# Kernel tuning notes

Hardware: AMD Instinct MI355X
Metric: run time of the kernel (lower is better)

The kernel has to match this reference:

```python
import jax, jax.numpy as jnp
import numpy as np

D_MODEL = 1024
N_HEADS = 16
HEAD_DIM = D_MODEL // N_HEADS
B, L = 2, 2048


def setup_inputs() -> dict:
    key = jax.random.key(0)
    ks = jax.random.split(key, 9)
    s = 1.0 / np.sqrt(D_MODEL)
    return {
        "hidden_states": jax.random.normal(ks[0], (B, L, D_MODEL), dtype=jnp.float32),
        "Wq": jax.random.uniform(ks[1], (D_MODEL, D_MODEL), jnp.float32, -s, s),
        "bq": jax.random.uniform(ks[2], (D_MODEL,), jnp.float32, -s, s),
        "Wk": jax.random.uniform(ks[3], (D_MODEL, D_MODEL), jnp.float32, -s, s),
        "bk": jax.random.uniform(ks[4], (D_MODEL,), jnp.float32, -s, s),
        "Wv": jax.random.uniform(ks[5], (D_MODEL, D_MODEL), jnp.float32, -s, s),
        "bv": jax.random.uniform(ks[6], (D_MODEL,), jnp.float32, -s, s),
        "Wo": jax.random.uniform(ks[7], (D_MODEL, D_MODEL), jnp.float32, -s, s),
        "bo": jax.random.uniform(ks[8], (D_MODEL,), jnp.float32, -s, s),
    }


def reference(hidden_states, Wq, bq, Wk, bk, Wv, bv, Wo, bo):
    b, l, d = hidden_states.shape
    h, hd = N_HEADS, HEAD_DIM
    scale = jnp.sqrt(jnp.asarray(hd, hidden_states.dtype))
    # projections (weights stored as [in, out], equivalent to torch Linear W.T)
    Q = (hidden_states @ Wq + bq).reshape(b, l, h, hd).transpose(0, 2, 1, 3)
    K = (hidden_states @ Wk + bk).reshape(b, l, h, hd).transpose(0, 2, 1, 3)
    V = (hidden_states @ Wv + bv).reshape(b, l, h, hd).transpose(0, 2, 1, 3)
    # [b, h, l, l] scores with causal mask
    scores = jnp.einsum("bhqd,bhkd->bhqk", Q, K) / scale
    causal = jnp.tril(jnp.ones((l, l), dtype=bool))
    scores = jnp.where(causal, scores, jnp.asarray(-jnp.inf, scores.dtype))
    weights = jax.nn.softmax(scores, axis=-1)
    out = jnp.einsum("bhqk,bhkd->bhqd", weights, V)
    out = out.transpose(0, 2, 1, 3).reshape(b, l, d)
    return out @ Wo + bo
```

## Files before the change

### kernel.cpp

```cpp
#include <hip/hip_runtime.h>

typedef unsigned short u16;
typedef unsigned int u32;
typedef __attribute__((ext_vector_type(8))) short bf16x8;
typedef __attribute__((ext_vector_type(4))) float f32x4;

__device__ __forceinline__ u16 f2bf(float f) {
    union { float f; u32 u; } x; x.f = f;
    u32 r = x.u + 0x7FFFu + ((x.u >> 16) & 1u);
    return (u16)(r >> 16);
}

__device__ __forceinline__ u16 f2bf_fast(float f) {
    union { float f; u32 u; } x; x.f = f;
    return (u16)((x.u + 0x8000u) >> 16);
}

__device__ __forceinline__ void gload16(const u16* g, u16* l) {
    __builtin_amdgcn_global_load_lds(
        (const __attribute__((address_space(1))) void*)g,
        (__attribute__((address_space(3))) void*)l,
        16, 0, 0);
}

__device__ __forceinline__ f32x4 mfma16(bf16x8 a, bf16x8 b, f32x4 c) {
    return __builtin_amdgcn_mfma_f32_16x16x32_bf16(a, b, c, 0, 0, 0);
}


__global__ __launch_bounds__(256) void cvt_x(const float* __restrict__ in, u16* __restrict__ out, int n4) {
    int i = blockIdx.x * blockDim.x + threadIdx.x;
    if (i >= n4) return;
    float4 v = ((const float4*)in)[i];
    u16* o = out + (size_t)i * 4;
    o[0] = f2bf(v.x); o[1] = f2bf(v.y); o[2] = f2bf(v.z); o[3] = f2bf(v.w);
}

__global__ __launch_bounds__(256) void transpose_w4(const float* __restrict__ Wq, const float* __restrict__ Wk,
                                                    const float* __restrict__ Wv, const float* __restrict__ Wo,
                                                    u16* __restrict__ qkvt, u16* __restrict__ wot) {
    __shared__ float tile[32][33];
    const float* in;
    u16* out;
    if (blockIdx.z == 0)      { in = Wq; out = qkvt; }
    else if (blockIdx.z == 1) { in = Wk; out = qkvt + 1024 * 1024; }
    else if (blockIdx.z == 2) { in = Wv; out = qkvt + 2 * 1024 * 1024; }
    else                      { in = Wo; out = wot; }
    const int bx = blockIdx.x * 32, by = blockIdx.y * 32;
    const int tx = threadIdx.x & 31, ty4 = (threadIdx.x >> 5) * 4;
#pragma unroll
    for (int j = 0; j < 4; ++j)
        tile[ty4 + j][tx] = in[(size_t)(by + ty4 + j) * 1024 + bx + tx];
    __syncthreads();
#pragma unroll
    for (int j = 0; j < 4; ++j)
        out[(size_t)(bx + ty4 + j) * 1024 + by + tx] = f2bf(tile[tx][ty4 + j]);
}

__global__ __launch_bounds__(256) void pack_bias(const float* __restrict__ bq, const float* __restrict__ bk,
                                                 const float* __restrict__ bv, float* __restrict__ out) {
    int i = blockIdx.x * blockDim.x + threadIdx.x;
    if (i >= 3072) return;
    out[i] = (i < 1024) ? bq[i] : ((i < 2048) ? bk[i - 1024] : bv[i - 2048]);
}

template<int MODE>
__global__ __launch_bounds__(256) void gemm128(const u16* __restrict__ A, const u16* __restrict__ Bt,
                                               const float* __restrict__ bias,
                                               u16* __restrict__ oq, u16* __restrict__ ok, u16* __restrict__ ov,
                                               float* __restrict__ of, int K)
{
    __shared__ u16 As[128 * 32];
    __shared__ u16 Bs[128 * 32];

    const int n0 = blockIdx.x * 128;
    const int m0 = blockIdx.y * 128;
    const int t = threadIdx.x;
    const int w = t >> 6, lane = t & 63;
    const int g = lane >> 4, lr = lane & 15;
    const int wm = w >> 1, wn = w & 1;
    const int srow = lane >> 2;
    const int scol = (lane & 3) * 8;

    f32x4 acc[4][4] = {};

    for (int k0 = 0; k0 < K; k0 += 32) {
        __syncthreads();
#pragma unroll
        for (int i = 0; i < 2; ++i) {
            const int c = w + i * 4;
            const int mrow = c * 16 + srow;
            gload16(A  + (size_t)(m0 + mrow) * K + k0 + scol, &As[c * 512 + lane * 8]);
            gload16(Bt + (size_t)(n0 + mrow) * K + k0 + scol, &Bs[c * 512 + lane * 8]);
        }
        __syncthreads();
        bf16x8 af[4], bfr[4];
#pragma unroll
        for (int mi = 0; mi < 4; ++mi) af[mi]  = *(const bf16x8*)&As[(wm * 64 + mi * 16 + lr) * 32 + g * 8];
#pragma unroll
        for (int ni = 0; ni < 4; ++ni) bfr[ni] = *(const bf16x8*)&Bs[(wn * 64 + ni * 16 + lr) * 32 + g * 8];
#pragma unroll
        for (int mi = 0; mi < 4; ++mi)
#pragma unroll
            for (int ni = 0; ni < 4; ++ni)
                acc[mi][ni] = mfma16(af[mi], bfr[ni], acc[mi][ni]);
    }

#pragma unroll
    for (int mi = 0; mi < 4; ++mi) {
#pragma unroll
        for (int ni = 0; ni < 4; ++ni) {
            const int col = n0 + wn * 64 + ni * 16 + lr;
            const int row0 = m0 + wm * 64 + mi * 16 + g * 4;
            const float bs = bias[col];
            if (MODE == 0) {
                const int mat = col >> 10;
                const int nn = col & 1023;
                const int h = nn >> 6, d = nn & 63;
#pragma unroll
                for (int j = 0; j < 4; ++j) {
                    const int rr = row0 + j;
                    const int b = rr >> 11, ll = rr & 2047;
                    const int bh = b * 16 + h;
                    const float v = acc[mi][ni][j] + bs;
                    if (mat == 0)      oq[((size_t)bh * 2048 + ll) * 64 + d] = f2bf(v * 0.1803368801111244f);
                    else if (mat == 1) ok[((size_t)bh * 2048 + ll) * 64 + d] = f2bf(v);
                    else               ov[((size_t)bh * 64 + d) * 2048 + ll] = f2bf(v);
                }
            } else {
#pragma unroll
                for (int j = 0; j < 4; ++j) {
                    const int rr = row0 + j;
                    of[(size_t)rr * 1024 + col] = acc[mi][ni][j] + bs;
                }
            }
        }
    }
}

__global__ __launch_bounds__(256) void attn(const u16* __restrict__ Q, const u16* __restrict__ Kg,
                                            const u16* __restrict__ Vt, u16* __restrict__ O)
{
    __shared__ u16 Ks[2][64 * 64];
    __shared__ u16 Vs[2][64 * 64];
    __shared__ u16 Ps[4][16 * 64];

    const int bh = blockIdx.x;
    const int qb = (int)gridDim.y - 1 - blockIdx.y;
    const int q0 = qb * 64;
    const int t = threadIdx.x;
    const int w = t >> 6, lane = t & 63;
    const int g = lane >> 4, lr = lane & 15;
    const int qw = q0 + w * 16;
    const int sw = lr & 7;

    const u16* Qb = Q  + (size_t)bh * 2048 * 64;
    const u16* Kb = Kg + (size_t)bh * 2048 * 64;
    const u16* Vb = Vt + (size_t)bh * 64 * 2048;

    const bf16x8 qf0 = *(const bf16x8*)&Qb[(size_t)(qw + lr) * 64 + g * 8];
    const bf16x8 qf1 = *(const bf16x8*)&Qb[(size_t)(qw + lr) * 64 + 32 + g * 8];

    const short one = (short)0x3F80;
    const bf16x8 vones = {one, one, one, one, one, one, one, one};

    f32x4 oacc[4] = {};
    f32x4 lsacc = {};
    float mrun[4];
#pragma unroll
    for (int j = 0; j < 4; ++j) mrun[j] = -1e30f;

    bf16x8 kreg[2], vreg[2];
    const int srow0 = t >> 3, sch = t & 7;
    auto issue = [&](int kb) {
#pragma unroll
        for (int i = 0; i < 2; ++i) {
            const int row = srow0 + i * 32;
            kreg[i] = *(const bf16x8*)&Kb[(size_t)(kb * 64 + row) * 64 + sch * 8];
            vreg[i] = *(const bf16x8*)&Vb[(size_t)row * 2048 + kb * 64 + sch * 8];
        }
    };
    auto commit = [&](int buf) {
#pragma unroll
        for (int i = 0; i < 2; ++i) {
            const int row = srow0 + i * 32;
            const int chs = sch ^ (row & 7);
            *(bf16x8*)&Ks[buf][row * 64 + chs * 8] = kreg[i];
            *(bf16x8*)&Vs[buf][row * 64 + chs * 8] = vreg[i];
        }
    };

    issue(0);
    commit(0);

    for (int kb = 0; kb <= qb; ++kb) {
        const int cur = kb & 1;
        const int k0 = kb * 64;
        __syncthreads();
        const bool more = (kb < qb);
        if (more) issue(kb + 1);

        f32x4 s[4] = {};
        __builtin_amdgcn_s_setprio(1);
#pragma unroll
        for (int ni = 0; ni < 4; ++ni) {
            const int row = ni * 16 + lr;
            bf16x8 kf0 = *(const bf16x8*)&Ks[cur][row * 64 + (g ^ sw) * 8];
            bf16x8 kf1 = *(const bf16x8*)&Ks[cur][row * 64 + ((4 + g) ^ sw) * 8];
            s[ni] = mfma16(qf0, kf0, s[ni]);
            s[ni] = mfma16(qf1, kf1, s[ni]);
        }
        __builtin_amdgcn_s_setprio(0);

        if (kb == qb) {
#pragma unroll
            for (int ni = 0; ni < 4; ++ni)
#pragma unroll
                for (int j = 0; j < 4; ++j)
                    if (k0 + ni * 16 + lr > qw + g * 4 + j) s[ni][j] = -1e30f;
        }

        float pm[4];
#pragma unroll
        for (int j = 0; j < 4; ++j) {
            float m0 = fmaxf(fmaxf(s[0][j], s[1][j]), fmaxf(s[2][j], s[3][j]));
            m0 = fmaxf(m0, __shfl_xor(m0, 1));
            m0 = fmaxf(m0, __shfl_xor(m0, 2));
            m0 = fmaxf(m0, __shfl_xor(m0, 4));
            m0 = fmaxf(m0, __shfl_xor(m0, 8));
            pm[j] = m0;
        }
        const bool need = (pm[0] > mrun[0] + 8.f) || (pm[1] > mrun[1] + 8.f) ||
                          (pm[2] > mrun[2] + 8.f) || (pm[3] > mrun[3] + 8.f);
        if (__any(need)) {
#pragma unroll
            for (int j = 0; j < 4; ++j) {
                const float mn = fmaxf(mrun[j], pm[j]);
                const float r = __builtin_amdgcn_exp2f(mrun[j] - mn);
                mrun[j] = mn;
                lsacc[j] *= r;
#pragma unroll
                for (int df = 0; df < 4; ++df) oacc[df][j] *= r;
            }
        }
#pragma unroll
        for (int j = 0; j < 4; ++j) {
            const int prow = g * 4 + j;
#pragma unroll
            for (int ni = 0; ni < 4; ++ni) {
                const float pv = __builtin_amdgcn_exp2f(s[ni][j] - mrun[j]);
                const int chunk = ni * 2 + (lr >> 3);
                Ps[w][prow * 64 + (chunk ^ (prow & 7)) * 8 + (lr & 7)] = f2bf_fast(pv);
            }
        }

        if (more) commit(cur ^ 1);

        const bf16x8 p0 = *(const bf16x8*)&Ps[w][lr * 64 + (g ^ sw) * 8];
        const bf16x8 p1 = *(const bf16x8*)&Ps[w][lr * 64 + ((4 + g) ^ sw) * 8];
        __builtin_amdgcn_s_setprio(1);
        lsacc = mfma16(p0, vones, lsacc);
        lsacc = mfma16(p1, vones, lsacc);
#pragma unroll
        for (int df = 0; df < 4; ++df) {
            const int row = df * 16 + lr;
            bf16x8 vf0 = *(const bf16x8*)&Vs[cur][row * 64 + (g ^ sw) * 8];
            bf16x8 vf1 = *(const bf16x8*)&Vs[cur][row * 64 + ((4 + g) ^ sw) * 8];
            oacc[df] = mfma16(p0, vf0, oacc[df]);
            oacc[df] = mfma16(p1, vf1, oacc[df]);
        }
        __builtin_amdgcn_s_setprio(0);
    }

    const int b = bh >> 4, h = bh & 15;
#pragma unroll
    for (int j = 0; j < 4; ++j) {
        const float inv = 1.f / lsacc[j];
        const int l = qw + g * 4 + j;
#pragma unroll
        for (int df = 0; df < 4; ++df)
            O[((size_t)b * 2048 + l) * 1024 + h * 64 + df * 16 + lr] = f2bf(oacc[df][j] * inv);
    }
}


extern "C" void kernel_launch(void* const* d_in, const int* in_sizes, int n_in,
                              void* d_out, int out_size, void* d_ws, size_t ws_size,
                              hipStream_t stream)
{
    const float* hs = (const float*)d_in[0];
    const float* Wq = (const float*)d_in[1];
    const float* bq = (const float*)d_in[2];
    const float* Wk = (const float*)d_in[3];
    const float* bk = (const float*)d_in[4];
    const float* Wv = (const float*)d_in[5];
    const float* bv = (const float*)d_in[6];
    const float* Wo = (const float*)d_in[7];
    const float* bo = (const float*)d_in[8];
    float* out = (float*)d_out;

    char* ws = (char*)d_ws;
    u16*   Xbf   = (u16*)(ws);
    u16*   Wqkvt = (u16*)(ws + (8ull  << 20));
    u16*   Wot   = (u16*)(ws + (14ull << 20));
    float* bqkv  = (float*)(ws + (16ull << 20));
    u16*   Qbuf  = (u16*)(ws + (17ull << 20));
    u16*   Kbuf  = (u16*)(ws + (25ull << 20));
    u16*   Vtbuf = (u16*)(ws + (33ull << 20));
    u16*   Abuf  = Xbf;

    cvt_x<<<4096, 256, 0, stream>>>(hs, Xbf, 4096 * 1024 / 4);
    transpose_w4<<<dim3(32, 32, 4), 256, 0, stream>>>(Wq, Wk, Wv, Wo, Wqkvt, Wot);
    pack_bias<<<12, 256, 0, stream>>>(bq, bk, bv, bqkv);

    gemm128<0><<<dim3(24, 32), 256, 0, stream>>>(Xbf, Wqkvt, bqkv, Qbuf, Kbuf, Vtbuf, nullptr, 1024);
    attn<<<dim3(32, 32), 256, 0, stream>>>(Qbuf, Kbuf, Vtbuf, Abuf);
    gemm128<1><<<dim3(8, 32), 256, 0, stream>>>(Abuf, Wot, bo, nullptr, nullptr, nullptr, out, 1024);
}
```

Measured before the change: 143.9 us.

## Transpose QK^T MFMA so each lane owns one query row's scores

Swaps the MFMA operand order so the score tile is transposed: each lane now holds scores for a single query row across several keys. The row max can then be taken mostly inside the lane with two cross-lane shuffles instead of four, and there is one running max per lane instead of four. Probabilities are packed in pairs into 32-bit LDS stores, halving the number of P writes. The rescale factor is redistributed to the output-accumulator layout with ds_bpermute, which adds a cross-lane permute on the rescale path.

```diff
diff --git a/kernel.cpp b/kernel.cpp
--- a/kernel.cpp
+++ b/kernel.cpp
@@ -166,9 +166,15 @@
 
     f32x4 oacc[4] = {};
     f32x4 lsacc = {};
-    float mrun[4];
-#pragma unroll
-    for (int j = 0; j < 4; ++j) mrun[j] = -1e30f;
+    float mrun = -1e30f;
+
+    int bpaddr[4];
+#pragma unroll
+    for (int j = 0; j < 4; ++j) bpaddr[j] = (20 * g + j) * 4;
+
+    const int pw_base = lr * 64;
+    const int g2h = g >> 1;
+    const int wic2 = (2 * g) & 3;
 
     bf16x8 kreg[2], vreg[2];
     const int srow0 = t >> 3, sch = t & 7;
@@ -207,50 +213,51 @@
             const int row = ni * 16 + lr;
             bf16x8 kf0 = *(const bf16x8*)&Ks[cur][row * 64 + (g ^ sw) * 8];
             bf16x8 kf1 = *(const bf16x8*)&Ks[cur][row * 64 + ((4 + g) ^ sw) * 8];
-            s[ni] = mfma16(qf0, kf0, s[ni]);
-            s[ni] = mfma16(qf1, kf1, s[ni]);
+            s[ni] = mfma16(kf0, qf0, s[ni]);
+            s[ni] = mfma16(kf1, qf1, s[ni]);
         }
         __builtin_amdgcn_s_setprio(0);
 
         if (kb == qb) {
+            const int qq = qw + lr;
 #pragma unroll
             for (int ni = 0; ni < 4; ++ni)
 #pragma unroll
                 for (int j = 0; j < 4; ++j)
-                    if (k0 + ni * 16 + lr > qw + g * 4 + j) s[ni][j] = -1e30f;
-        }
-
-        float pm[4];
-#pragma unroll
-        for (int j = 0; j < 4; ++j) {
-            float m0 = fmaxf(fmaxf(s[0][j], s[1][j]), fmaxf(s[2][j], s[3][j]));
-            m0 = fmaxf(m0, __shfl_xor(m0, 1));
-            m0 = fmaxf(m0, __shfl_xor(m0, 2));
-            m0 = fmaxf(m0, __shfl_xor(m0, 4));
-            m0 = fmaxf(m0, __shfl_xor(m0, 8));
-            pm[j] = m0;
-        }
-        const bool need = (pm[0] > mrun[0] + 8.f) || (pm[1] > mrun[1] + 8.f) ||
-                          (pm[2] > mrun[2] + 8.f) || (pm[3] > mrun[3] + 8.f);
-        if (__any(need)) {
+                    if (k0 + ni * 16 + g * 4 + j > qq) s[ni][j] = -1e30f;
+        }
+
+        float pm = fmaxf(fmaxf(fmaxf(s[0][0], s[0][1]), fmaxf(s[0][2], s[0][3])),
+                         fmaxf(fmaxf(s[1][0], s[1][1]), fmaxf(s[1][2], s[1][3])));
+        pm = fmaxf(pm, fmaxf(fmaxf(fmaxf(s[2][0], s[2][1]), fmaxf(s[2][2], s[2][3])),
+                             fmaxf(fmaxf(s[3][0], s[3][1]), fmaxf(s[3][2], s[3][3]))));
+        pm = fmaxf(pm, __shfl_xor(pm, 16));
+        pm = fmaxf(pm, __shfl_xor(pm, 32));
+
+        if (__any(pm > mrun + 8.f)) {
+            const float mn = fmaxf(mrun, pm);
+            const float r = __builtin_amdgcn_exp2f(mrun - mn);
+            mrun = mn;
+            const int ri = __float_as_int(r);
 #pragma unroll
             for (int j = 0; j < 4; ++j) {
-                const float mn = fmaxf(mrun[j], pm[j]);
-                const float r = __builtin_amdgcn_exp2f(mrun[j] - mn);
-                mrun[j] = mn;
-                lsacc[j] *= r;
-#pragma unroll
-                for (int df = 0; df < 4; ++df) oacc[df][j] *= r;
+                const float ro = __int_as_float(__builtin_amdgcn_ds_bpermute(bpaddr[j], ri));
+                lsacc[j] *= ro;
+#pragma unroll
+                for (int df = 0; df < 4; ++df) oacc[df][j] *= ro;
             }
         }
-#pragma unroll
-        for (int j = 0; j < 4; ++j) {
-            const int prow = g * 4 + j;
-#pragma unroll
-            for (int ni = 0; ni < 4; ++ni) {
-                const float pv = __builtin_amdgcn_exp2f(s[ni][j] - mrun[j]);
-                const int chunk = ni * 2 + (lr >> 3);
-                Ps[w][prow * 64 + (chunk ^ (prow & 7)) * 8 + (lr & 7)] = f2bf_fast(pv);
+
+#pragma unroll
+        for (int ni = 0; ni < 4; ++ni) {
+            const int c8 = 2 * ni + g2h;
+#pragma unroll
+            for (int jp = 0; jp < 2; ++jp) {
+                const float plo = __builtin_amdgcn_exp2f(s[ni][2 * jp]     - mrun);
+                const float phi = __builtin_amdgcn_exp2f(s[ni][2 * jp + 1] - mrun);
+                const u32 pr = (u32)f2bf_fast(plo) | ((u32)f2bf_fast(phi) << 16);
+                const int wic = wic2 + jp;
+                *(u32*)&Ps[w][pw_base + (c8 ^ sw) * 8 + wic * 2] = pr;
             }
         }
 
```

After: 134.9 us. 1.07x faster.
